# Performance work log

Hardware: AMD Instinct MI355X
Metric: run time of the kernel (lower is better)

## Reference

```python
import jax, jax.numpy as jnp
import numpy as np
from jax import lax

S = 30      # num_sensors
FD = 200    # feature_dim
T = 1024    # signal length
B = 1024    # batch
NC = 7      # num_classes


def setup_inputs() -> dict:
    key = jax.random.key(0)
    ks = jax.random.split(key, 24)
    rn = lambda i, shape: jax.random.normal(ks[i], shape, jnp.float32) * 0.05
    # normalized adjacency with self-loops: D^-1/2 (A+I) D^-1/2
    rng = np.random.default_rng(0)
    A = (rng.random((S, S)) > 0.7).astype(np.float32)
    A = ((A + A.T) > 0).astype(np.float32)
    A_self = A + np.eye(S, dtype=np.float32)
    dinv = 1.0 / np.sqrt(A_self.sum(1))
    adj_self = jnp.asarray(dinv[:, None] * A_self * dinv[None, :])
    return dict(
        x=jax.random.normal(ks[0], (B, S, T), jnp.float32),
        adj_self=adj_self,
        Wc1=rn(1, (S, S, 3)), bc1=jnp.zeros((S,), jnp.float32),
        Wc2=rn(2, (S, S, 3)), bc2=jnp.zeros((S,), jnp.float32),
        Wt=rn(3, (T, FD)), bt=jnp.zeros((FD,), jnp.float32),
        Wa=rn(4, (FD, FD)),
        Wm1=rn(5, (FD, FD)), Wm2=rn(6, (FD, FD)), Wm3=rn(7, (FD, FD)),
        Wg1=rn(8, (FD, FD)), Wg2=rn(9, (FD, FD)),
        wg=rn(10, (FD, 3)),
        Wp1=rn(11, (FD, FD // 2)), Wp2=rn(12, (FD, FD // 2)), Wp3=rn(13, (FD, FD // 2)),
        Wl=rn(14, (FD, 150)), Wgl=rn(15, (FD, 150)),
        Ws1=rn(16, (S, S // 2)), Ws2=rn(17, (S // 2, S)),
        Wf1=rn(18, (300, 150)), Wf2=rn(19, (150, 300)),
        Wcls=rn(20, (S * 600, NC)), bcls=jnp.zeros((NC,), jnp.float32),
    )


def reference(x, adj_self, Wc1, bc1, Wc2, bc2, Wt, bt, Wa, Wm1, Wm2, Wm3,
              Wg1, Wg2, wg, Wp1, Wp2, Wp3, Wl, Wgl, Ws1, Ws2, Wf1, Wf2,
              Wcls, bcls):
    dn = ('NCH', 'OIH', 'NCH')
    # CNN feature extractor: [B,S,T] -> [B,S,FD]
    h = jax.nn.relu(lax.conv_general_dilated(x, Wc1, (1,), 'SAME', dimension_numbers=dn) + bc1[None, :, None])
    h = jax.nn.relu(lax.conv_general_dilated(h, Wc2, (1,), 'SAME', dimension_numbers=dn) + bc2[None, :, None])
    F2 = jax.nn.relu(jnp.einsum('bst,tf->bsf', h, Wt) + bt)
    # MGCN: learned feature adjacency + 3-order GCN (batched, replaces per-sample loop)
    A_F = jax.nn.softmax(jax.nn.relu(jnp.einsum('bif,fg,bjg->bij', F2, Wa, F2)), axis=-1)
    gc = lambda A, X, W: jax.nn.relu(jnp.einsum('bij,bjf,fg->big', A, X, W))
    x1 = gc(A_F, F2, Wm1)
    x2 = gc(A_F, x1, Wm2)
    x3 = gc(A_F, x2, Wm3)
    # signal GCN on physical adjacency (2-layer, eval mode so dropout is identity)
    h1 = jax.nn.relu(jnp.einsum('ij,bjf,fg->big', adj_self, F2, Wg1))
    x_sensor = jnp.einsum('ij,bjf,fg->big', adj_self, h1, Wg2)
    H1 = (x1 + x_sensor) * 0.5
    H2 = (x2 + x_sensor) * 0.5
    H3 = (x3 + x_sensor) * 0.5
    # adaptive aggregation: per-node softmax gate over 3 branches, project to FD//2 each -> 300
    scores = jnp.stack([jnp.einsum('bsf,f->bs', H, wg[:, k]) for k, H in enumerate((H1, H2, H3))], -1)
    g = jax.nn.softmax(scores, -1)  # [B,S,3]
    agg = lambda k, H, Wp: jnp.einsum('ij,bjf,fg->big', adj_self, g[..., k:k + 1] * H, Wp)
    G_h = jnp.concatenate([agg(0, H1, Wp1), agg(1, H2, Wp2), agg(2, H3, Wp3)], -1)  # [B,S,300]
    # LGFM: local (physical adj) + global (learned adj) -> 150+150
    loc = jax.nn.relu(jnp.einsum('ij,bjf,fg->big', adj_self, F2, Wl))
    glb = jax.nn.relu(jnp.einsum('bij,bjf,fg->big', A_F, F2, Wgl))
    G_v = jnp.concatenate([loc, glb], -1)  # [B,S,300]
    # cross squeeze-excitation: channel SE on G_h driven by G_v, feature SE on G_v driven by G_h
    wch = jax.nn.sigmoid(jax.nn.relu(G_v.mean(-1) @ Ws1) @ Ws2)   # [B,S]
    G_h_att = G_h * wch[:, :, None]
    wft = jax.nn.sigmoid(jax.nn.relu(G_h.mean(1) @ Wf1) @ Wf2)    # [B,300]
    G_v_att = G_v * wft[:, None, :]
    G = jnp.concatenate([G_h_att, G_v_att], -1).reshape(x.shape[0], -1)  # [B, S*600]
    return jax.nn.log_softmax(G @ Wcls + bcls, axis=-1)
```

## Files before the change

### kernel.cpp

```cpp
#include <hip/hip_runtime.h>
#include <math.h>

#define S   30
#define FD  200
#define TT  1024
#define BB  1024
#define NC  7

#define OFS_C1   0ull
#define OFS_F2   31457280ull
#define OFS_AF   0ull
#define OFS_GV   921600ull
#define OFS_GH   10137600ull
#define OFS_WCH  19353600ull
#define OFS_WFT  19384320ull

__global__ __launch_bounds__(256) void k_conv1(
    const float* __restrict__ x,
    const float* __restrict__ Wc1, const float* __restrict__ bc1,
    float* __restrict__ C1) {
    const int c = blockIdx.x, b = blockIdx.y;
    const int t = threadIdx.x;
    const int t0 = c * 256;
    __shared__ float xb[S * 258];
    __shared__ float w1l[90 * 32];
    for (int idx = t; idx < 2700; idx += 256) {
        int so = idx / 90, r = idx % 90;
        w1l[r * 32 + so] = Wc1[idx];
    }
    for (int idx = t; idx < 180; idx += 256) {
        int r = idx >> 1, z = idx & 1;
        w1l[r * 32 + 30 + z] = 0.f;
    }
    for (int idx = t; idx < S * 64; idx += 256) {
        int s = idx >> 6, u = idx & 63;
        float4 v = *(const float4*)(x + (size_t)(b * S + s) * TT + t0 + 4 * u);
        float* d = xb + s * 258 + 1 + 4 * u;
        d[0] = v.x; d[1] = v.y; d[2] = v.z; d[3] = v.w;
    }
    if (t < 60) {
        int s = t % S;
        if (t < S) {
            int gt = t0 - 1;
            xb[s * 258] = (gt >= 0) ? x[(size_t)(b * S + s) * TT + gt] : 0.f;
        } else {
            int gt = t0 + 256;
            xb[s * 258 + 257] = (gt < TT) ? x[(size_t)(b * S + s) * TT + gt] : 0.f;
        }
    }
    __syncthreads();
    float acc[32];
#pragma unroll
    for (int so = 0; so < 32; so++) acc[so] = (so < S) ? bc1[so] : 0.f;
    for (int si = 0; si < S; si++) {
        float v0 = xb[si * 258 + t];
        float v1 = xb[si * 258 + t + 1];
        float v2 = xb[si * 258 + t + 2];
        const float* wr = w1l + si * 96;
#pragma unroll
        for (int u = 0; u < 8; u++) {
            float4 w0 = *(const float4*)(wr + 4 * u);
            float4 w1 = *(const float4*)(wr + 32 + 4 * u);
            float4 w2 = *(const float4*)(wr + 64 + 4 * u);
            acc[4 * u + 0] = fmaf(w0.x, v0, fmaf(w1.x, v1, fmaf(w2.x, v2, acc[4 * u + 0])));
            acc[4 * u + 1] = fmaf(w0.y, v0, fmaf(w1.y, v1, fmaf(w2.y, v2, acc[4 * u + 1])));
            acc[4 * u + 2] = fmaf(w0.z, v0, fmaf(w1.z, v1, fmaf(w2.z, v2, acc[4 * u + 2])));
            acc[4 * u + 3] = fmaf(w0.w, v0, fmaf(w1.w, v1, fmaf(w2.w, v2, acc[4 * u + 3])));
        }
    }
#pragma unroll
    for (int so = 0; so < 32; so++) {
        if (so < S)
            C1[(size_t)(b * S + so) * TT + t0 + t] = fmaxf(acc[so], 0.f);
    }
}

#define FMA4(av, wv, accm)                           \
    {                                                \
        accm[0] = fmaf(av, (wv).x, accm[0]);         \
        accm[1] = fmaf(av, (wv).y, accm[1]);         \
        accm[2] = fmaf(av, (wv).z, accm[2]);         \
        accm[3] = fmaf(av, (wv).w, accm[3]);         \
    }

__device__ inline void fma_tile8(const float4 a0, const float4 a1,
                                 const float4 w[8], float accm[4]) {
    FMA4(a0.x, w[0], accm); FMA4(a0.y, w[1], accm);
    FMA4(a0.z, w[2], accm); FMA4(a0.w, w[3], accm);
    FMA4(a1.x, w[4], accm); FMA4(a1.y, w[5], accm);
    FMA4(a1.z, w[6], accm); FMA4(a1.w, w[7], accm);
}

template<int RPT>
__device__ inline void zacc(float acc[][4]) {
#pragma unroll
    for (int m = 0; m < RPT; m++)
#pragma unroll
        for (int q = 0; q < 4; q++) acc[m][q] = 0.f;
}

template<int RPT, int N, int K>
__device__ inline void gemm_w4_pf(const float* Xl, int xstr, const float* __restrict__ W,
                                  int ct, int rt, float acc[][4]) {
    const float* wp = W + 4 * ct;
    float4 wreg[8];
#pragma unroll
    for (int u = 0; u < 8; u++) wreg[u] = *(const float4*)(wp + u * N);
#pragma unroll 1
    for (int kt = 0; kt < K / 8 - 1; kt++) {
        float4 wnxt[8];
#pragma unroll
        for (int u = 0; u < 8; u++) wnxt[u] = *(const float4*)(wp + (kt * 8 + 8 + u) * N);
#pragma unroll
        for (int m = 0; m < RPT; m++) {
            const float* xr = Xl + (rt * RPT + m) * xstr + kt * 8;
            float4 a0 = *(const float4*)(xr);
            float4 a1 = *(const float4*)(xr + 4);
            fma_tile8(a0, a1, wreg, acc[m]);
        }
#pragma unroll
        for (int u = 0; u < 8; u++) wreg[u] = wnxt[u];
    }
    {
        const int kb = K - 8;
#pragma unroll
        for (int m = 0; m < RPT; m++) {
            const float* xr = Xl + (rt * RPT + m) * xstr + kb;
            float4 a0 = *(const float4*)(xr);
            float4 a1 = *(const float4*)(xr + 4);
            fma_tile8(a0, a1, wreg, acc[m]);
        }
    }
}

template<int RPT>
__device__ inline void gemm_a32(const float* Al, const float* Xl, int xstr,
                                int ct, int rt, float acc[][4]) {
#pragma unroll
    for (int k4 = 0; k4 < 8; k4++) {
        float4 xv0 = *(const float4*)(Xl + (4 * k4 + 0) * xstr + 4 * ct);
        float4 xv1 = *(const float4*)(Xl + (4 * k4 + 1) * xstr + 4 * ct);
        float4 xv2 = *(const float4*)(Xl + (4 * k4 + 2) * xstr + 4 * ct);
        float4 xv3 = *(const float4*)(Xl + (4 * k4 + 3) * xstr + 4 * ct);
#pragma unroll
        for (int m = 0; m < RPT; m++) {
            float4 av = *(const float4*)(Al + (rt * RPT + m) * 32 + 4 * k4);
            FMA4(av.x, xv0, acc[m]);
            FMA4(av.y, xv1, acc[m]);
            FMA4(av.z, xv2, acc[m]);
            FMA4(av.w, xv3, acc[m]);
        }
    }
}

__device__ inline void gemm_w150_pf(const float* Xl, const float* __restrict__ W,
                                    int ct2, int rt2, float acc[5][4], int off23) {
    const float* wp = W + 4 * ct2;
    float2 wa[8], wb[8];
#pragma unroll
    for (int u = 0; u < 8; u++) {
        wa[u] = *(const float2*)(wp + u * 150);
        wb[u] = *(const float2*)(wp + u * 150 + off23);
    }
#pragma unroll 1
    for (int kt = 0; kt < 24; kt++) {
        float2 na[8], nb[8];
#pragma unroll
        for (int u = 0; u < 8; u++) {
            int k = kt * 8 + 8 + u;
            na[u] = *(const float2*)(wp + k * 150);
            nb[u] = *(const float2*)(wp + k * 150 + off23);
        }
#pragma unroll
        for (int m = 0; m < 5; m++) {
            const float* xr = Xl + (rt2 * 5 + m) * FD + kt * 8;
            float4 a0 = *(const float4*)(xr);
            float4 a1 = *(const float4*)(xr + 4);
            float av[8] = {a0.x, a0.y, a0.z, a0.w, a1.x, a1.y, a1.z, a1.w};
#pragma unroll
            for (int u = 0; u < 8; u++) {
                acc[m][0] = fmaf(av[u], wa[u].x, acc[m][0]);
                acc[m][1] = fmaf(av[u], wa[u].y, acc[m][1]);
                acc[m][2] = fmaf(av[u], wb[u].x, acc[m][2]);
                acc[m][3] = fmaf(av[u], wb[u].y, acc[m][3]);
            }
        }
#pragma unroll
        for (int u = 0; u < 8; u++) { wa[u] = na[u]; wb[u] = nb[u]; }
    }
#pragma unroll
    for (int m = 0; m < 5; m++) {
        const float* xr = Xl + (rt2 * 5 + m) * FD + 192;
        float4 a0 = *(const float4*)(xr);
        float4 a1 = *(const float4*)(xr + 4);
        float av[8] = {a0.x, a0.y, a0.z, a0.w, a1.x, a1.y, a1.z, a1.w};
#pragma unroll
        for (int u = 0; u < 8; u++) {
            acc[m][0] = fmaf(av[u], wa[u].x, acc[m][0]);
            acc[m][1] = fmaf(av[u], wa[u].y, acc[m][1]);
            acc[m][2] = fmaf(av[u], wb[u].x, acc[m][2]);
            acc[m][3] = fmaf(av[u], wb[u].y, acc[m][3]);
        }
    }
}

__global__ __launch_bounds__(256) void k_f2(
    const float* __restrict__ C1,
    const float* __restrict__ Wc2, const float* __restrict__ bc2,
    const float* __restrict__ Wt, const float* __restrict__ bt,
    float* __restrict__ F2) {
    const int b = blockIdx.x, t = threadIdx.x;
    __shared__ float buf[S * 130];
    __shared__ float w2l[90 * 32];
    const int ct = t % 50, rt = t / 50;
    const int c3p = t & 63, sg = t >> 6;
    const int p0 = 2 * c3p;

    for (int idx = t; idx < 2700; idx += 256) {
        int ch = idx / 90, r = idx % 90;
        w2l[r * 32 + ch] = Wc2[idx];
    }
    for (int idx = t; idx < 180; idx += 256) {
        int r = idx >> 1, z = idx & 1;
        w2l[r * 32 + 30 + z] = 0.f;
    }
    float bias[8];
#pragma unroll
    for (int m = 0; m < 8; m++) {
        int ch = sg * 8 + m;
        bias[m] = bc2[ch < S ? ch : 0];
    }
    float acc[6][4];
    zacc<6>(acc);

    for (int ks = 0; ks < 8; ks++) {
        for (int idx = t; idx < S * 32; idx += 256) {
            int s = idx >> 5, u = idx & 31;
            float4 v = *(const float4*)(C1 + (size_t)(b * S + s) * TT + ks * 128 + 4 * u);
            float* d = buf + s * 130 + 1 + 4 * u;
            d[0] = v.x; d[1] = v.y; d[2] = v.z; d[3] = v.w;
        }
        if (t < 60) {
            int s = t % S;
            if (t < S) {
                int gt = ks * 128 - 1;
                buf[s * 130] = (gt >= 0) ? C1[(size_t)(b * S + s) * TT + gt] : 0.f;
            } else {
                int gt = ks * 128 + 128;
                buf[s * 130 + 129] = (gt < TT) ? C1[(size_t)(b * S + s) * TT + gt] : 0.f;
            }
        }
        __syncthreads();
        float a0[8], a1[8];
#pragma unroll
        for (int m = 0; m < 8; m++) { a0[m] = bias[m]; a1[m] = bias[m]; }
        for (int si = 0; si < S; si++) {
            float2 va = *(const float2*)(buf + si * 130 + p0);
            float2 vb = *(const float2*)(buf + si * 130 + p0 + 2);
            const float* wr = w2l + si * 96 + sg * 8;
            float4 w0a = *(const float4*)(wr);
            float4 w0b = *(const float4*)(wr + 4);
            float4 w1a = *(const float4*)(wr + 32);
            float4 w1b = *(const float4*)(wr + 36);
            float4 w2a = *(const float4*)(wr + 64);
            float4 w2b = *(const float4*)(wr + 68);
            float w0[8] = {w0a.x, w0a.y, w0a.z, w0a.w, w0b.x, w0b.y, w0b.z, w0b.w};
            float w1[8] = {w1a.x, w1a.y, w1a.z, w1a.w, w1b.x, w1b.y, w1b.z, w1b.w};
            float w2[8] = {w2a.x, w2a.y, w2a.z, w2a.w, w2b.x, w2b.y, w2b.z, w2b.w};
#pragma unroll
            for (int m = 0; m < 8; m++) {
                a0[m] = fmaf(w0[m], va.x, fmaf(w1[m], va.y, fmaf(w2[m], vb.x, a0[m])));
                a1[m] = fmaf(w0[m], va.y, fmaf(w1[m], vb.x, fmaf(w2[m], vb.y, a1[m])));
            }
        }
        __syncthreads();
#pragma unroll
        for (int m = 0; m < 8; m++) {
            int ch = sg * 8 + m;
            if (ch < S) {
                float2 o = {fmaxf(a0[m], 0.f), fmaxf(a1[m], 0.f)};
                *(float2*)(buf + ch * 128 + p0) = o;
            }
        }
        __syncthreads();
        if (t < 250)
            gemm_w4_pf<6, FD, 128>(buf, 128, Wt + (size_t)ks * 128 * FD, ct, rt, acc);
        __syncthreads();
    }
    if (t < 250) {
#pragma unroll
        for (int m = 0; m < 6; m++) {
            int row = rt * 6 + m;
            float4 o;
            o.x = fmaxf(acc[m][0] + bt[4 * ct + 0], 0.f);
            o.y = fmaxf(acc[m][1] + bt[4 * ct + 1], 0.f);
            o.z = fmaxf(acc[m][2] + bt[4 * ct + 2], 0.f);
            o.w = fmaxf(acc[m][3] + bt[4 * ct + 3], 0.f);
            *(float4*)(F2 + (size_t)(b * S + row) * FD + 4 * ct) = o;
        }
    }
}

__global__ __launch_bounds__(256) void k_att(
    const float* __restrict__ F2, const float* __restrict__ Wa,
    const float* __restrict__ adj, const float* __restrict__ Wl,
    const float* __restrict__ Wgl,
    float* __restrict__ AF, float* __restrict__ Gv) {
    const int b = blockIdx.x, t = threadIdx.x;
    __shared__ float A[32 * FD];
    __shared__ float Bu[32 * FD];
    __shared__ float scl[32 * 32];
    __shared__ float adjl[32 * 32];
    for (int idx = t; idx < 32 * FD; idx += 256) {
        A[idx] = (idx < S * FD) ? F2[(size_t)b * S * FD + idx] : 0.f;
        if (idx >= S * FD) Bu[idx] = 0.f;
    }
    for (int idx = t; idx < 1024; idx += 256) {
        int r = idx >> 5, cc = idx & 31;
        adjl[idx] = (r < S && cc < S) ? adj[r * S + cc] : 0.f;
        scl[idx] = 0.f;
    }
    __syncthreads();
    const int ct = t % 50, rt = t / 50;
    float acc[6][4];
    zacc<6>(acc);
    if (t < 250) {
        gemm_w4_pf<6, FD, FD>(A, FD, Wa, ct, rt, acc);
#pragma unroll
        for (int m = 0; m < 6; m++) {
            float4 o = {acc[m][0], acc[m][1], acc[m][2], acc[m][3]};
            *(float4*)(Bu + (rt * 6 + m) * FD + 4 * ct) = o;
        }
    }
    __syncthreads();
    for (int idx = t; idx < S * S; idx += 256) {
        int i = idx / S, j = idx % S;
        float a = 0.f;
        for (int f4 = 0; f4 < 50; f4++) {
            float4 p = *(const float4*)(Bu + i * FD + 4 * f4);
            float4 q = *(const float4*)(A + j * FD + 4 * f4);
            a = fmaf(p.x, q.x, a); a = fmaf(p.y, q.y, a);
            a = fmaf(p.z, q.z, a); a = fmaf(p.w, q.w, a);
        }
        scl[i * 32 + j] = fmaxf(a, 0.f);
    }
    __syncthreads();
    if (t < S) {
        float mx = -1e30f;
        for (int j = 0; j < S; j++) mx = fmaxf(mx, scl[t * 32 + j]);
        float den = 0.f;
        for (int j = 0; j < S; j++) den += expf(scl[t * 32 + j] - mx);
        float inv = 1.f / den;
        for (int j = 0; j < S; j++) scl[t * 32 + j] = expf(scl[t * 32 + j] - mx) * inv;
    }
    __syncthreads();
    for (int idx = t; idx < S * S; idx += 256)
        AF[(size_t)b * S * S + idx] = scl[(idx / S) * 32 + (idx % S)];
    zacc<6>(acc);
    if (t < 250) gemm_a32<6>(adjl, A, FD, ct, rt, acc);
    __syncthreads();
    if (t < 250)
#pragma unroll
        for (int m = 0; m < 6; m++) {
            float4 o = {acc[m][0], acc[m][1], acc[m][2], acc[m][3]};
            *(float4*)(Bu + (rt * 6 + m) * FD + 4 * ct) = o;
        }
    __syncthreads();
    const int ct2 = t % 38, rt2 = t / 38;
    const bool full = (4 * ct2 + 2) < 150;
    const int off23 = full ? 2 : -2;
    if (t < 228) {
        float a2[5][4];
        zacc<5>(a2);
        gemm_w150_pf(Bu, Wl, ct2, rt2, a2, off23);
#pragma unroll
        for (int m = 0; m < 5; m++) {
            float* o = Gv + (size_t)(b * S + rt2 * 5 + m) * 300 + 4 * ct2;
            o[0] = fmaxf(a2[m][0], 0.f); o[1] = fmaxf(a2[m][1], 0.f);
            if (full) { o[2] = fmaxf(a2[m][2], 0.f); o[3] = fmaxf(a2[m][3], 0.f); }
        }
    }
    __syncthreads();
    zacc<6>(acc);
    if (t < 250) gemm_a32<6>(scl, A, FD, ct, rt, acc);
    __syncthreads();
    if (t < 250)
#pragma unroll
        for (int m = 0; m < 6; m++) {
            float4 o = {acc[m][0], acc[m][1], acc[m][2], acc[m][3]};
            *(float4*)(Bu + (rt * 6 + m) * FD + 4 * ct) = o;
        }
    __syncthreads();
    if (t < 228) {
        float a2[5][4];
        zacc<5>(a2);
        gemm_w150_pf(Bu, Wgl, ct2, rt2, a2, off23);
#pragma unroll
        for (int m = 0; m < 5; m++) {
            float* o = Gv + (size_t)(b * S + rt2 * 5 + m) * 300 + 150 + 4 * ct2;
            o[0] = fmaxf(a2[m][0], 0.f); o[1] = fmaxf(a2[m][1], 0.f);
            if (full) { o[2] = fmaxf(a2[m][2], 0.f); o[3] = fmaxf(a2[m][3], 0.f); }
        }
    }
}

__global__ __launch_bounds__(256) void k_mgcn(
    const float* __restrict__ F2, const float* __restrict__ AF,
    const float* __restrict__ adj,
    const float* __restrict__ Wg1, const float* __restrict__ Wg2,
    const float* __restrict__ Wm1, const float* __restrict__ Wm2,
    const float* __restrict__ Wm3, const float* __restrict__ wg,
    const float* __restrict__ Wp1, const float* __restrict__ Wp2,
    const float* __restrict__ Wp3, float* __restrict__ Gh) {
    const int b = blockIdx.x, t = threadIdx.x;
    __shared__ float A[32 * FD];
    __shared__ float Bu[32 * FD];
    __shared__ float afl[32 * 32];
    __shared__ float adjl[32 * 32];
    __shared__ float sk[96];
    __shared__ float gl[96];
    const int ct = t % 50, rt = t / 50;
    const int ct3 = t % 25, rt3 = t / 25;
    for (int idx = t; idx < 32 * FD; idx += 256) {
        A[idx] = (idx < S * FD) ? F2[(size_t)b * S * FD + idx] : 0.f;
        if (idx >= S * FD) Bu[idx] = 0.f;
    }
    for (int idx = t; idx < 1024; idx += 256) {
        int r = idx >> 5, cc = idx & 31;
        afl[idx] = (r < S && cc < S) ? AF[(size_t)b * S * S + r * S + cc] : 0.f;
        adjl[idx] = (r < S && cc < S) ? adj[r * S + cc] : 0.f;
    }
    if (t < 96) sk[t] = 0.f;
    __syncthreads();

    float acc[6][4];
#define STAGE_A(AL, XIN, XOUT)                                              \
    {                                                                       \
        zacc<6>(acc);                                                       \
        if (t < 250) gemm_a32<6>(AL, XIN, FD, ct, rt, acc);                 \
        __syncthreads();                                                    \
        if (t < 250) {                                                      \
            _Pragma("unroll")                                               \
            for (int m = 0; m < 6; m++) {                                   \
                float4 o = {acc[m][0], acc[m][1], acc[m][2], acc[m][3]};    \
                *(float4*)(XOUT + (rt * 6 + m) * FD + 4 * ct) = o;          \
            }                                                               \
        }                                                                   \
        __syncthreads();                                                    \
    }
#define STAGE_W(XIN, W, XOUT, RELU)                                         \
    {                                                                       \
        zacc<6>(acc);                                                       \
        if (t < 250) gemm_w4_pf<6, FD, FD>(XIN, FD, W, ct, rt, acc);        \
        __syncthreads();                                                    \
        if (t < 250) {                                                      \
            _Pragma("unroll")                                               \
            for (int m = 0; m < 6; m++) {                                   \
                float4 o;                                                   \
                o.x = RELU ? fmaxf(acc[m][0], 0.f) : acc[m][0];             \
                o.y = RELU ? fmaxf(acc[m][1], 0.f) : acc[m][1];             \
                o.z = RELU ? fmaxf(acc[m][2], 0.f) : acc[m][2];             \
                o.w = RELU ? fmaxf(acc[m][3], 0.f) : acc[m][3];             \
                *(float4*)(XOUT + (rt * 6 + m) * FD + 4 * ct) = o;          \
            }                                                               \
        }                                                                   \
        __syncthreads();                                                    \
    }

    STAGE_A(adjl, A, Bu);
    STAGE_W(Bu, Wg1, Bu, true);
    STAGE_A(adjl, Bu, Bu);
    STAGE_W(Bu, Wg2, Bu, false);

    float h1r[6][4], h2r[6][4], h3r[6][4];
#define EXTRACT_H(HR, K)                                                    \
    {                                                                       \
        if (t < 250) {                                                      \
            _Pragma("unroll")                                               \
            for (int m = 0; m < 6; m++) {                                   \
                int row = rt * 6 + m;                                       \
                float4 xv = *(const float4*)(A + row * FD + 4 * ct);        \
                float4 sv = *(const float4*)(Bu + row * FD + 4 * ct);       \
                HR[m][0] = 0.5f * (xv.x + sv.x);                            \
                HR[m][1] = 0.5f * (xv.y + sv.y);                            \
                HR[m][2] = 0.5f * (xv.z + sv.z);                            \
                HR[m][3] = 0.5f * (xv.w + sv.w);                            \
                float p = HR[m][0] * wg[(4 * ct + 0) * 3 + K]               \
                        + HR[m][1] * wg[(4 * ct + 1) * 3 + K]               \
                        + HR[m][2] * wg[(4 * ct + 2) * 3 + K]               \
                        + HR[m][3] * wg[(4 * ct + 3) * 3 + K];              \
                atomicAdd(&sk[row * 3 + K], p);                             \
            }                                                               \
        }                                                                   \
        __syncthreads();                                                    \
    }

    STAGE_A(afl, A, A);
    STAGE_W(A, Wm1, A, true);
    EXTRACT_H(h1r, 0);
    STAGE_A(afl, A, A);
    STAGE_W(A, Wm2, A, true);
    EXTRACT_H(h2r, 1);
    STAGE_A(afl, A, A);
    STAGE_W(A, Wm3, A, true);
    EXTRACT_H(h3r, 2);

    if (t < S) {
        float a0 = sk[t * 3 + 0], a1 = sk[t * 3 + 1], a2 = sk[t * 3 + 2];
        float m = fmaxf(a0, fmaxf(a1, a2));
        float e0 = expf(a0 - m), e1 = expf(a1 - m), e2 = expf(a2 - m);
        float inv = 1.f / (e0 + e1 + e2);
        gl[t * 3 + 0] = e0 * inv; gl[t * 3 + 1] = e1 * inv; gl[t * 3 + 2] = e2 * inv;
    }
    __syncthreads();

#define GH_STAGE(HR, K, WP)                                                 \
    {                                                                       \
        if (t < 250) {                                                      \
            _Pragma("unroll")                                               \
            for (int m = 0; m < 6; m++) {                                   \
                float4 o = {HR[m][0], HR[m][1], HR[m][2], HR[m][3]};        \
                *(float4*)(A + (rt * 6 + m) * FD + 4 * ct) = o;             \
            }                                                               \
        }                                                                   \
        for (int idx = t; idx < 1024; idx += 256) {                         \
            int cc = idx & 31;                                              \
            afl[idx] = (cc < S) ? adjl[idx] * gl[cc * 3 + K] : 0.f;         \
        }                                                                   \
        __syncthreads();                                                    \
        STAGE_A(afl, A, Bu);                                                \
        if (t < 250) {                                                      \
            float a3[3][4];                                                 \
            zacc<3>(a3);                                                    \
            gemm_w4_pf<3, 100, FD>(Bu, FD, WP, ct3, rt3, a3);               \
            _Pragma("unroll")                                               \
            for (int m = 0; m < 3; m++) {                                   \
                float4 o = {a3[m][0], a3[m][1], a3[m][2], a3[m][3]};        \
                *(float4*)(Gh + (size_t)(b * S + rt3 * 3 + m) * 300 + K * 100 + 4 * ct3) = o; \
            }                                                               \
        }                                                                   \
        __syncthreads();                                                    \
    }
    GH_STAGE(h1r, 0, Wp1);
    GH_STAGE(h2r, 1, Wp2);
    GH_STAGE(h3r, 2, Wp3);
#undef STAGE_A
#undef STAGE_W
#undef EXTRACT_H
#undef GH_STAGE
}

__global__ __launch_bounds__(256) void k_se(const float* __restrict__ Gv, const float* __restrict__ Gh,
                                            const float* __restrict__ Ws1, const float* __restrict__ Ws2,
                                            const float* __restrict__ Wf1, const float* __restrict__ Wf2,
                                            float* __restrict__ wch, float* __restrict__ wft) {
    int b = blockIdx.x, t = threadIdx.x;
    __shared__ float mrow[S];
    __shared__ float u[15];
    __shared__ float mb[300];
    __shared__ float v[150];
    if (t < S) {
        float a = 0.f;
        const float* gp = Gv + ((size_t)b * S + t) * 300;
        for (int j = 0; j < 300; j++) a += gp[j];
        mrow[t] = a * (1.f / 300.f);
    }
    for (int j = t; j < 300; j += 256) {
        float a = 0.f;
        for (int s = 0; s < S; s++) a += Gh[(size_t)b * S * 300 + s * 300 + j];
        mb[j] = a * (1.f / S);
    }
    __syncthreads();
    if (t < 15) {
        float a = 0.f;
        for (int i = 0; i < S; i++) a += mrow[i] * Ws1[i * 15 + t];
        u[t] = fmaxf(a, 0.f);
    }
    if (t >= 64 && t < 64 + 150) {
        int h = t - 64;
        float a = 0.f;
        for (int j = 0; j < 300; j++) a += mb[j] * Wf1[j * 150 + h];
        v[h] = fmaxf(a, 0.f);
    }
    __syncthreads();
    if (t < S) {
        float a = 0.f;
        for (int h = 0; h < 15; h++) a += u[h] * Ws2[h * 30 + t];
        wch[b * S + t] = 1.f / (1.f + expf(-a));
    }
    for (int j = t; j < 300; j += 256) {
        float a = 0.f;
        for (int h = 0; h < 150; h++) a += v[h] * Wf2[h * 300 + j];
        wft[b * 300 + j] = 1.f / (1.f + expf(-a));
    }
}

__global__ __launch_bounds__(256) void k_cls(const float* __restrict__ Gh, const float* __restrict__ Gv,
                                             const float* __restrict__ wch, const float* __restrict__ wft,
                                             const float* __restrict__ Wcls, const float* __restrict__ bcls,
                                             float* __restrict__ out) {
    const int b = blockIdx.x, t = threadIdx.x;
    __shared__ float red[NC][256];
    __shared__ float wftl[300];
    __shared__ float wchl[S];
    for (int j = t; j < 300; j += 256) wftl[j] = wft[(size_t)b * 300 + j];
    if (t < S) wchl[t] = wch[b * S + t];
    __syncthreads();
    float acc[NC];
#pragma unroll
    for (int c = 0; c < NC; c++) acc[c] = 0.f;
    for (int i = t; i < S * 600; i += 256) {
        int s = i / 600, j = i % 600;
        float gval = (j < 300)
            ? Gh[(size_t)b * S * 300 + s * 300 + j] * wchl[s]
            : Gv[(size_t)b * S * 300 + s * 300 + (j - 300)] * wftl[j - 300];
        const float* wr = Wcls + (size_t)i * NC;
#pragma unroll
        for (int c = 0; c < NC; c++) acc[c] = fmaf(gval, wr[c], acc[c]);
    }
#pragma unroll
    for (int c = 0; c < NC; c++) red[c][t] = acc[c];
    __syncthreads();
    for (int off = 128; off > 0; off >>= 1) {
        if (t < off) {
#pragma unroll
            for (int c = 0; c < NC; c++) red[c][t] += red[c][t + off];
        }
        __syncthreads();
    }
    if (t == 0) {
        float lg[NC];
        float mx = -1e30f;
#pragma unroll
        for (int c = 0; c < NC; c++) { lg[c] = red[c][0] + bcls[c]; mx = fmaxf(mx, lg[c]); }
        float den = 0.f;
#pragma unroll
        for (int c = 0; c < NC; c++) den += expf(lg[c] - mx);
        float lden = logf(den) + mx;
#pragma unroll
        for (int c = 0; c < NC; c++) out[b * NC + c] = lg[c] - lden;
    }
}

extern "C" void kernel_launch(void* const* d_in, const int* in_sizes, int n_in,
                              void* d_out, int out_size, void* d_ws, size_t ws_size,
                              hipStream_t stream) {
    const float* x    = (const float*)d_in[0];
    const float* adj  = (const float*)d_in[1];
    const float* Wc1  = (const float*)d_in[2];
    const float* bc1  = (const float*)d_in[3];
    const float* Wc2  = (const float*)d_in[4];
    const float* bc2  = (const float*)d_in[5];
    const float* Wt   = (const float*)d_in[6];
    const float* bt   = (const float*)d_in[7];
    const float* Wa   = (const float*)d_in[8];
    const float* Wm1  = (const float*)d_in[9];
    const float* Wm2  = (const float*)d_in[10];
    const float* Wm3  = (const float*)d_in[11];
    const float* Wg1  = (const float*)d_in[12];
    const float* Wg2  = (const float*)d_in[13];
    const float* wg   = (const float*)d_in[14];
    const float* Wp1  = (const float*)d_in[15];
    const float* Wp2  = (const float*)d_in[16];
    const float* Wp3  = (const float*)d_in[17];
    const float* Wl   = (const float*)d_in[18];
    const float* Wgl  = (const float*)d_in[19];
    const float* Ws1  = (const float*)d_in[20];
    const float* Ws2  = (const float*)d_in[21];
    const float* Wf1  = (const float*)d_in[22];
    const float* Wf2  = (const float*)d_in[23];
    const float* Wcls = (const float*)d_in[24];
    const float* bcls = (const float*)d_in[25];

    float* ws  = (float*)d_ws;
    float* C1  = ws + OFS_C1;
    float* F2  = ws + OFS_F2;
    float* AF  = ws + OFS_AF;
    float* GV  = ws + OFS_GV;
    float* GH  = ws + OFS_GH;
    float* WCH = ws + OFS_WCH;
    float* WFT = ws + OFS_WFT;
    float* out = (float*)d_out;

    k_conv1<<<dim3(4, BB), 256, 0, stream>>>(x, Wc1, bc1, C1);
    k_f2<<<BB, 256, 0, stream>>>(C1, Wc2, bc2, Wt, bt, F2);
    k_att<<<BB, 256, 0, stream>>>(F2, Wa, adj, Wl, Wgl, AF, GV);
    k_mgcn<<<BB, 256, 0, stream>>>(F2, AF, adj, Wg1, Wg2, Wm1, Wm2, Wm3, wg,
                                   Wp1, Wp2, Wp3, GH);
    k_se<<<BB, 256, 0, stream>>>(GV, GH, Ws1, Ws2, Wf1, Wf2, WCH, WFT);
    k_cls<<<BB, 256, 0, stream>>>(GH, GV, WCH, WFT, Wcls, bcls, out);
}
```

Baseline: 1.150 ms.

## Drop second shared buffer in MGCN kernel, reorder Wp projection before gated aggregation

The MGCN kernel loses its second 32x200 shared buffer so that more blocks fit per CU (launch bounds now request 4). The three H branches are no longer held in registers. Each branch's Wp projection is applied first and spilled to a global workspace, then the gate-scaled adjacency is applied afterwards on the narrower 100-wide result, using associativity. The sensor-branch result is held in registers and F2 is reloaded from global memory. The trade is extra global traffic and extra workspace in exchange for lower LDS and register pressure.

```diff
diff --git a/kernel.cpp b/kernel.cpp
--- a/kernel.cpp
+++ b/kernel.cpp
@@ -14,6 +14,7 @@
 #define OFS_GH   10137600ull
 #define OFS_WCH  19353600ull
 #define OFS_WFT  19384320ull
+#define OFS_R    19691520ull
 
 __global__ __launch_bounds__(256) void k_conv1(
     const float* __restrict__ x,
@@ -404,106 +405,129 @@
     }
 }
 
-__global__ __launch_bounds__(256) void k_mgcn(
-    const float* __restrict__ F2, const float* __restrict__ AF,
+__global__ __launch_bounds__(256, 4) void k_mgcn(
+    const float* __restrict__ F2g, const float* __restrict__ AFg,
     const float* __restrict__ adj,
     const float* __restrict__ Wg1, const float* __restrict__ Wg2,
     const float* __restrict__ Wm1, const float* __restrict__ Wm2,
     const float* __restrict__ Wm3, const float* __restrict__ wg,
     const float* __restrict__ Wp1, const float* __restrict__ Wp2,
-    const float* __restrict__ Wp3, float* __restrict__ Gh) {
+    const float* __restrict__ Wp3,
+    float* __restrict__ Rws, float* __restrict__ Gh) {
     const int b = blockIdx.x, t = threadIdx.x;
     __shared__ float A[32 * FD];
-    __shared__ float Bu[32 * FD];
     __shared__ float afl[32 * 32];
     __shared__ float adjl[32 * 32];
     __shared__ float sk[96];
     __shared__ float gl[96];
     const int ct = t % 50, rt = t / 50;
     const int ct3 = t % 25, rt3 = t / 25;
-    for (int idx = t; idx < 32 * FD; idx += 256) {
-        A[idx] = (idx < S * FD) ? F2[(size_t)b * S * FD + idx] : 0.f;
-        if (idx >= S * FD) Bu[idx] = 0.f;
-    }
+
+    for (int idx = t; idx < 1500; idx += 256)
+        *(float4*)(A + 4 * idx) = *(const float4*)(F2g + (size_t)b * S * FD + 4 * idx);
+    for (int idx = t; idx < 400; idx += 256) A[6000 + idx] = 0.f;
     for (int idx = t; idx < 1024; idx += 256) {
         int r = idx >> 5, cc = idx & 31;
-        afl[idx] = (r < S && cc < S) ? AF[(size_t)b * S * S + r * S + cc] : 0.f;
+        afl[idx] = (r < S && cc < S) ? AFg[(size_t)b * S * S + r * S + cc] : 0.f;
         adjl[idx] = (r < S && cc < S) ? adj[r * S + cc] : 0.f;
     }
     if (t < 96) sk[t] = 0.f;
     __syncthreads();
 
     float acc[6][4];
-#define STAGE_A(AL, XIN, XOUT)                                              \
-    {                                                                       \
-        zacc<6>(acc);                                                       \
-        if (t < 250) gemm_a32<6>(AL, XIN, FD, ct, rt, acc);                 \
-        __syncthreads();                                                    \
-        if (t < 250) {                                                      \
-            _Pragma("unroll")                                               \
-            for (int m = 0; m < 6; m++) {                                   \
-                float4 o = {acc[m][0], acc[m][1], acc[m][2], acc[m][3]};    \
-                *(float4*)(XOUT + (rt * 6 + m) * FD + 4 * ct) = o;          \
-            }                                                               \
+    float xsr[6][4];
+
+#define WRITE_ACC_A(RELU)                                                   \
+    if (t < 250) {                                                          \
+        _Pragma("unroll")                                                   \
+        for (int m = 0; m < 6; m++) {                                       \
+            float4 o;                                                       \
+            o.x = RELU ? fmaxf(acc[m][0], 0.f) : acc[m][0];                 \
+            o.y = RELU ? fmaxf(acc[m][1], 0.f) : acc[m][1];                 \
+            o.z = RELU ? fmaxf(acc[m][2], 0.f) : acc[m][2];                 \
+            o.w = RELU ? fmaxf(acc[m][3], 0.f) : acc[m][3];                 \
+            *(float4*)(A + (rt * 6 + m) * FD + 4 * ct) = o;                 \
         }                                                                   \
-        __syncthreads();                                                    \
-    }
-#define STAGE_W(XIN, W, XOUT, RELU)                                         \
-    {                                                                       \
-        zacc<6>(acc);                                                       \
-        if (t < 250) gemm_w4_pf<6, FD, FD>(XIN, FD, W, ct, rt, acc);        \
-        __syncthreads();                                                    \
-        if (t < 250) {                                                      \
-            _Pragma("unroll")                                               \
-            for (int m = 0; m < 6; m++) {                                   \
-                float4 o;                                                   \
-                o.x = RELU ? fmaxf(acc[m][0], 0.f) : acc[m][0];             \
-                o.y = RELU ? fmaxf(acc[m][1], 0.f) : acc[m][1];             \
-                o.z = RELU ? fmaxf(acc[m][2], 0.f) : acc[m][2];             \
-                o.w = RELU ? fmaxf(acc[m][3], 0.f) : acc[m][3];             \
-                *(float4*)(XOUT + (rt * 6 + m) * FD + 4 * ct) = o;          \
-            }                                                               \
-        }                                                                   \
-        __syncthreads();                                                    \
-    }
-
-    STAGE_A(adjl, A, Bu);
-    STAGE_W(Bu, Wg1, Bu, true);
-    STAGE_A(adjl, Bu, Bu);
-    STAGE_W(Bu, Wg2, Bu, false);
-
-    float h1r[6][4], h2r[6][4], h3r[6][4];
-#define EXTRACT_H(HR, K)                                                    \
-    {                                                                       \
-        if (t < 250) {                                                      \
-            _Pragma("unroll")                                               \
-            for (int m = 0; m < 6; m++) {                                   \
-                int row = rt * 6 + m;                                       \
-                float4 xv = *(const float4*)(A + row * FD + 4 * ct);        \
-                float4 sv = *(const float4*)(Bu + row * FD + 4 * ct);       \
-                HR[m][0] = 0.5f * (xv.x + sv.x);                            \
-                HR[m][1] = 0.5f * (xv.y + sv.y);                            \
-                HR[m][2] = 0.5f * (xv.z + sv.z);                            \
-                HR[m][3] = 0.5f * (xv.w + sv.w);                            \
-                float p = HR[m][0] * wg[(4 * ct + 0) * 3 + K]               \
-                        + HR[m][1] * wg[(4 * ct + 1) * 3 + K]               \
-                        + HR[m][2] * wg[(4 * ct + 2) * 3 + K]               \
-                        + HR[m][3] * wg[(4 * ct + 3) * 3 + K];              \
-                atomicAdd(&sk[row * 3 + K], p);                             \
-            }                                                               \
-        }                                                                   \
-        __syncthreads();                                                    \
-    }
-
-    STAGE_A(afl, A, A);
-    STAGE_W(A, Wm1, A, true);
-    EXTRACT_H(h1r, 0);
-    STAGE_A(afl, A, A);
-    STAGE_W(A, Wm2, A, true);
-    EXTRACT_H(h2r, 1);
-    STAGE_A(afl, A, A);
-    STAGE_W(A, Wm3, A, true);
-    EXTRACT_H(h3r, 2);
+    }
+
+    zacc<6>(acc);
+    if (t < 250) gemm_a32<6>(adjl, A, FD, ct, rt, acc);
+    __syncthreads();
+    WRITE_ACC_A(false);
+    __syncthreads();
+    zacc<6>(acc);
+    if (t < 250) gemm_w4_pf<6, FD, FD>(A, FD, Wg1, ct, rt, acc);
+    __syncthreads();
+    WRITE_ACC_A(true);
+    __syncthreads();
+    zacc<6>(acc);
+    if (t < 250) gemm_a32<6>(adjl, A, FD, ct, rt, acc);
+    __syncthreads();
+    WRITE_ACC_A(false);
+    __syncthreads();
+    zacc<6>(acc);
+    if (t < 250) gemm_w4_pf<6, FD, FD>(A, FD, Wg2, ct, rt, acc);
+    __syncthreads();
+#pragma unroll
+    for (int m = 0; m < 6; m++) {
+#pragma unroll
+        for (int q = 0; q < 4; q++) xsr[m][q] = acc[m][q];
+    }
+    for (int idx = t; idx < 1500; idx += 256)
+        *(float4*)(A + 4 * idx) = *(const float4*)(F2g + (size_t)b * S * FD + 4 * idx);
+    __syncthreads();
+
+    const float* Wm[3] = {Wm1, Wm2, Wm3};
+    const float* Wp[3] = {Wp1, Wp2, Wp3};
+#pragma unroll 1
+    for (int k = 0; k < 3; k++) {
+        zacc<6>(acc);
+        if (t < 250) gemm_a32<6>(afl, A, FD, ct, rt, acc);
+        __syncthreads();
+        WRITE_ACC_A(false);
+        __syncthreads();
+        zacc<6>(acc);
+        if (t < 250) gemm_w4_pf<6, FD, FD>(A, FD, Wm[k], ct, rt, acc);
+        __syncthreads();
+        if (t < 250) {
+#pragma unroll
+            for (int m = 0; m < 6; m++) {
+#pragma unroll
+                for (int q = 0; q < 4; q++) acc[m][q] = fmaxf(acc[m][q], 0.f);
+            }
+#pragma unroll
+            for (int m = 0; m < 6; m++) {
+                int row = rt * 6 + m;
+                float h0 = 0.5f * (acc[m][0] + xsr[m][0]);
+                float h1 = 0.5f * (acc[m][1] + xsr[m][1]);
+                float h2 = 0.5f * (acc[m][2] + xsr[m][2]);
+                float h3 = 0.5f * (acc[m][3] + xsr[m][3]);
+                float4 o = {h0, h1, h2, h3};
+                *(float4*)(A + row * FD + 4 * ct) = o;
+                float p = h0 * wg[(4 * ct + 0) * 3 + k]
+                        + h1 * wg[(4 * ct + 1) * 3 + k]
+                        + h2 * wg[(4 * ct + 2) * 3 + k]
+                        + h3 * wg[(4 * ct + 3) * 3 + k];
+                atomicAdd(&sk[row * 3 + k], p);
+            }
+        }
+        __syncthreads();
+        if (t < 250) {
+            float a3[3][4];
+            zacc<3>(a3);
+            gemm_w4_pf<3, 100, FD>(A, FD, Wp[k], ct3, rt3, a3);
+#pragma unroll
+            for (int m = 0; m < 3; m++) {
+                float4 o = {a3[m][0], a3[m][1], a3[m][2], a3[m][3]};
+                *(float4*)(Rws + ((size_t)(k * BB + b) * S + rt3 * 3 + m) * 100 + 4 * ct3) = o;
+            }
+        }
+        __syncthreads();
+        if (k < 2) {
+            WRITE_ACC_A(false);
+            __syncthreads();
+        }
+    }
 
     if (t < S) {
         float a0 = sk[t * 3 + 0], a1 = sk[t * 3 + 1], a2 = sk[t * 3 + 2];
@@ -514,40 +538,30 @@
     }
     __syncthreads();
 
-#define GH_STAGE(HR, K, WP)                                                 \
-    {                                                                       \
-        if (t < 250) {                                                      \
-            _Pragma("unroll")                                               \
-            for (int m = 0; m < 6; m++) {                                   \
-                float4 o = {HR[m][0], HR[m][1], HR[m][2], HR[m][3]};        \
-                *(float4*)(A + (rt * 6 + m) * FD + 4 * ct) = o;             \
-            }                                                               \
-        }                                                                   \
-        for (int idx = t; idx < 1024; idx += 256) {                         \
-            int cc = idx & 31;                                              \
-            afl[idx] = (cc < S) ? adjl[idx] * gl[cc * 3 + K] : 0.f;         \
-        }                                                                   \
-        __syncthreads();                                                    \
-        STAGE_A(afl, A, Bu);                                                \
-        if (t < 250) {                                                      \
-            float a3[3][4];                                                 \
-            zacc<3>(a3);                                                    \
-            gemm_w4_pf<3, 100, FD>(Bu, FD, WP, ct3, rt3, a3);               \
-            _Pragma("unroll")                                               \
-            for (int m = 0; m < 3; m++) {                                   \
-                float4 o = {a3[m][0], a3[m][1], a3[m][2], a3[m][3]};        \
-                *(float4*)(Gh + (size_t)(b * S + rt3 * 3 + m) * 300 + K * 100 + 4 * ct3) = o; \
-            }                                                               \
-        }                                                                   \
-        __syncthreads();                                                    \
-    }
-    GH_STAGE(h1r, 0, Wp1);
-    GH_STAGE(h2r, 1, Wp2);
-    GH_STAGE(h3r, 2, Wp3);
-#undef STAGE_A
-#undef STAGE_W
-#undef EXTRACT_H
-#undef GH_STAGE
+#pragma unroll 1
+    for (int k = 0; k < 3; k++) {
+        for (int idx = t; idx < S * 100; idx += 256) {
+            int row = idx / 100, col = idx % 100;
+            A[row * FD + col] = Rws[((size_t)(k * BB + b) * S) * 100 + idx];
+        }
+        for (int idx = t; idx < 1024; idx += 256) {
+            int cc = idx & 31;
+            afl[idx] = (cc < S) ? adjl[idx] * gl[cc * 3 + k] : 0.f;
+        }
+        __syncthreads();
+        if (t < 250) {
+            float a3[3][4];
+            zacc<3>(a3);
+            gemm_a32<3>(afl, A, FD, ct3, rt3, a3);
+#pragma unroll
+            for (int m = 0; m < 3; m++) {
+                float4 o = {a3[m][0], a3[m][1], a3[m][2], a3[m][3]};
+                *(float4*)(Gh + (size_t)(b * S + rt3 * 3 + m) * 300 + k * 100 + 4 * ct3) = o;
+            }
+        }
+        __syncthreads();
+    }
+#undef WRITE_ACC_A
 }
 
 __global__ __launch_bounds__(256) void k_se(const float* __restrict__ Gv, const float* __restrict__ Gh,
@@ -680,13 +694,14 @@
     float* GH  = ws + OFS_GH;
     float* WCH = ws + OFS_WCH;
     float* WFT = ws + OFS_WFT;
+    float* RWS = ws + OFS_R;
     float* out = (float*)d_out;
 
     k_conv1<<<dim3(4, BB), 256, 0, stream>>>(x, Wc1, bc1, C1);
     k_f2<<<BB, 256, 0, stream>>>(C1, Wc2, bc2, Wt, bt, F2);
     k_att<<<BB, 256, 0, stream>>>(F2, Wa, adj, Wl, Wgl, AF, GV);
     k_mgcn<<<BB, 256, 0, stream>>>(F2, AF, adj, Wg1, Wg2, Wm1, Wm2, Wm3, wg,
-                                   Wp1, Wp2, Wp3, GH);
+                                   Wp1, Wp2, Wp3, RWS, GH);
     k_se<<<BB, 256, 0, stream>>>(GV, GH, Ws1, Ws2, Wf1, Wf2, WCH, WFT);
     k_cls<<<BB, 256, 0, stream>>>(GH, GV, WCH, WFT, Wcls, bcls, out);
 }
```

After: 1.148 ms. No clear change (-0.2%).
